# Performance work log

Hardware: AMD Instinct MI355X
Metric: run time of the kernel (lower is better)

The kernel has to match this reference:

```python
import jax, jax.numpy as jnp
import numpy as np

N = 50000      # nodes
E = 800000     # edges (avg degree 16)
C = 5000       # clusters (Kongming compression)
D = 128        # in_features
OUT = 40       # out_features (classes)
K = 2          # propagation hops


def setup_inputs() -> dict:
    key = jax.random.key(0)
    k1, k2, k3, k4, k5, k6 = jax.random.split(key, 6)
    x = jax.random.normal(k1, (N, D), dtype=jnp.float32)
    edge_index = jax.random.randint(k2, (2, E), 0, N, dtype=jnp.int32)
    cluster_index = jax.random.randint(k3, (N,), 0, C, dtype=jnp.int32)
    rep_idx = jax.random.randint(k4, (C,), 0, N, dtype=jnp.int32)
    W = jax.random.normal(k5, (OUT, D), dtype=jnp.float32) / np.sqrt(D)
    b = jax.random.normal(k6, (OUT,), dtype=jnp.float32) * 0.01
    return {"x": x, "edge_index": edge_index, "cluster_index": cluster_index,
            "rep_idx": rep_idx, "W": W, "b": b}


def _gcn_propagate(x, edge_index, k_hops):
    # PUPropagate: K hops of D^{-1/2}(A+I)D^{-1/2} x (gcn_norm with self-loops)
    n = x.shape[0]
    loops = jnp.arange(n, dtype=edge_index.dtype)
    src = jnp.concatenate([edge_index[0], loops])
    dst = jnp.concatenate([edge_index[1], loops])
    deg = jax.ops.segment_sum(jnp.ones_like(src, dtype=x.dtype), dst, num_segments=n)
    dinv = jnp.where(deg > 0, jax.lax.rsqrt(deg), 0.0)
    norm = (dinv[src] * dinv[dst])[:, None]            # [E+N, 1]
    h = x
    for _ in range(k_hops):                            # small fixed hop count
        h = jax.ops.segment_sum(h[src] * norm, dst, num_segments=n)
    return h


def reference(x, edge_index, cluster_index, rep_idx, W, b):
    h = _gcn_propagate(x, edge_index, K)               # [N, D]
    # Kongming_Cluster: gather one representative row per cluster
    hc = h[rep_idx]                                    # [C, D]
    yc = hc @ W.T + b                                  # [C, OUT] dense linear on compressed rows
    # Kongming_Reconstruct: scatter back to all nodes by cluster index
    y = yc[cluster_index]                              # [N, OUT]
    return jax.nn.log_softmax(y, axis=1)
```

## Files before the change

### kernel.cpp

```cpp
#include <hip/hip_runtime.h>
#include <math.h>

#define N_NODES 50000
#define N_EDGES 800000
#define N_CLUST 5000
#define DIM     128
#define NOUT    40
#define SLOTS   64
#define CSLOT   64

#define NBKT    391
#define BCAP    2560
#define GB_STR  16
#define BUCKB   250
#define EPB4    800

#define ZB     782
#define INVB   50
#define GRID_A (ZB + INVB + BUCKB)

typedef __attribute__((ext_vector_type(8))) short short8;
typedef __attribute__((ext_vector_type(4))) float fvec4;
typedef __attribute__((ext_vector_type(4))) int ivec4;
typedef __attribute__((ext_vector_type(4))) unsigned uvec4;

__device__ __forceinline__ short bf16r(float v) {
    unsigned u = __float_as_uint(v);
    u = (u + 0x7FFFu + ((u >> 16) & 1u)) >> 16;
    return (short)u;
}
__device__ __forceinline__ unsigned pack_bf16x2(float a, float b) {
    unsigned ua = __float_as_uint(a);
    unsigned ub = __float_as_uint(b);
    ua = (ua + 0x7FFFu + ((ua >> 16) & 1u)) >> 16;
    ub = (ub + 0x7FFFu + ((ub >> 16) & 1u)) >> 16;
    return ua | (ub << 16);
}
__device__ __forceinline__ float2 unpack_bf16x2(unsigned v) {
    float2 r;
    r.x = __uint_as_float(v << 16);
    r.y = __uint_as_float(v & 0xFFFF0000u);
    return r;
}
__device__ __forceinline__ float4 unpack_bf16x4(uint2 v) {
    float4 r;
    r.x = __uint_as_float(v.x << 16);
    r.y = __uint_as_float(v.x & 0xFFFF0000u);
    r.z = __uint_as_float(v.y << 16);
    r.w = __uint_as_float(v.y & 0xFFFF0000u);
    return r;
}
struct f8 { float4 a, b; };
__device__ __forceinline__ f8 unpack_bf16x8(uint4 q) {
    f8 r;
    r.a.x = __uint_as_float(q.x << 16);
    r.a.y = __uint_as_float(q.x & 0xFFFF0000u);
    r.a.z = __uint_as_float(q.y << 16);
    r.a.w = __uint_as_float(q.y & 0xFFFF0000u);
    r.b.x = __uint_as_float(q.z << 16);
    r.b.y = __uint_as_float(q.z & 0xFFFF0000u);
    r.b.z = __uint_as_float(q.w << 16);
    r.b.w = __uint_as_float(q.w & 0xFFFF0000u);
    return r;
}
__device__ __forceinline__ float4 sel4(bool c, float4 v) {
    float4 r;
    r.x = c ? v.x : 0.0f; r.y = c ? v.y : 0.0f;
    r.z = c ? v.z : 0.0f; r.w = c ? v.w : 0.0f;
    return r;
}

__global__ __launch_bounds__(256) void fused_A(const float* __restrict__ x,
                                               const int* __restrict__ esrc,
                                               const int* __restrict__ edst,
                                               const int* __restrict__ cidx,
                                               const float* __restrict__ W,
                                               int* __restrict__ ccnt,
                                               unsigned short* __restrict__ zs,
                                               unsigned short* __restrict__ cinv,
                                               int* __restrict__ gbcnt,
                                               unsigned* __restrict__ gbuck) {
    __shared__ int bcnt[NBKT];
    __shared__ int bbase[NBKT];
    int lane = threadIdx.x & 63;
    int wv = threadIdx.x >> 6;

    if (blockIdx.x < ZB) {
        int gw = blockIdx.x * 4 + wv;
        if (gw >= N_NODES / 16) return;
        int q = lane >> 4, r16 = lane & 15;

        short8 bfr[3][4];
        #pragma unroll
        for (int t = 0; t < 3; t++) {
            int o = t * 16 + r16;
            #pragma unroll
            for (int s = 0; s < 4; s++) {
                short8 f = {0, 0, 0, 0, 0, 0, 0, 0};
                if (o < NOUT) {
                    const float* wp = W + o * DIM + s * 32 + q * 8;
                    float4 w0 = *(const float4*)wp;
                    float4 w1 = *(const float4*)(wp + 4);
                    f[0] = bf16r(w0.x); f[1] = bf16r(w0.y);
                    f[2] = bf16r(w0.z); f[3] = bf16r(w0.w);
                    f[4] = bf16r(w1.x); f[5] = bf16r(w1.y);
                    f[6] = bf16r(w1.z); f[7] = bf16r(w1.w);
                }
                bfr[t][s] = f;
            }
        }

        int tile = gw;
        int node = tile * 16 + r16;
        short8 af[4];
        #pragma unroll
        for (int s = 0; s < 4; s++) {
            const fvec4* xp = (const fvec4*)(x + (size_t)node * DIM + s * 32 + q * 8);
            fvec4 a0 = *xp;
            fvec4 a1 = *(xp + 1);
            short8 f;
            f[0] = bf16r(a0.x); f[1] = bf16r(a0.y);
            f[2] = bf16r(a0.z); f[3] = bf16r(a0.w);
            f[4] = bf16r(a1.x); f[5] = bf16r(a1.y);
            f[6] = bf16r(a1.z); f[7] = bf16r(a1.w);
            af[s] = f;
        }

        fvec4 acc0 = {0, 0, 0, 0}, acc1 = {0, 0, 0, 0}, acc2 = {0, 0, 0, 0};
        #pragma unroll
        for (int s = 0; s < 4; s++) {
            acc0 = __builtin_amdgcn_mfma_f32_16x16x32_bf16(af[s], bfr[0][s], acc0, 0, 0, 0);
            acc1 = __builtin_amdgcn_mfma_f32_16x16x32_bf16(af[s], bfr[1][s], acc1, 0, 0, 0);
            acc2 = __builtin_amdgcn_mfma_f32_16x16x32_bf16(af[s], bfr[2][s], acc2, 0, 0, 0);
        }

        #pragma unroll
        for (int r = 0; r < 4; r++) {
            int nd = tile * 16 + q * 4 + r;
            unsigned short* zrow = zs + (size_t)nd * NOUT;
            zrow[r16] = (unsigned short)bf16r(acc0[r]);
            zrow[16 + r16] = (unsigned short)bf16r(acc1[r]);
            if (r16 < 8)
                zrow[32 + r16] = (unsigned short)bf16r(acc2[r]);
        }
    } else if (blockIdx.x < ZB + INVB) {
        int t0 = (blockIdx.x - ZB) * 256 + threadIdx.x;
        for (int i = t0; i < N_NODES; i += INVB * 256) {
            int c = cidx[i];
            int pos = atomicAdd(&ccnt[c], 1);
            if (pos < CSLOT) cinv[c * CSLOT + pos] = (unsigned short)i;
        }
    } else {
        int fb = blockIdx.x - ZB - INVB;
        const ivec4* src4 = (const ivec4*)esrc;
        const ivec4* dst4 = (const ivec4*)edst;
        int q0 = fb * EPB4;

        for (int i = threadIdx.x; i < NBKT; i += 256) bcnt[i] = 0;
        __syncthreads();

        for (int i = threadIdx.x; i < EPB4; i += 256) {
            ivec4 d4 = dst4[q0 + i];
            atomicAdd(&bcnt[d4.x >> 7], 1);
            atomicAdd(&bcnt[d4.y >> 7], 1);
            atomicAdd(&bcnt[d4.z >> 7], 1);
            atomicAdd(&bcnt[d4.w >> 7], 1);
        }
        __syncthreads();

        for (int bk = threadIdx.x; bk < NBKT; bk += 256) {
            int c = bcnt[bk];
            bbase[bk] = c ? atomicAdd(&gbcnt[bk * GB_STR], c) : 0;
        }
        __syncthreads();
        for (int i = threadIdx.x; i < NBKT; i += 256) bcnt[i] = 0;
        __syncthreads();

        for (int i = threadIdx.x; i < EPB4; i += 256) {
            ivec4 d4 = dst4[q0 + i];
            ivec4 s4 = src4[q0 + i];
            {
                int bk = d4.x >> 7; int idx = atomicAdd(&bcnt[bk], 1);
                unsigned p = (unsigned)(bbase[bk] + idx);
                if (p < BCAP) gbuck[(size_t)bk * BCAP + p] = ((unsigned)d4.x << 16) | (unsigned)s4.x;
            }
            {
                int bk = d4.y >> 7; int idx = atomicAdd(&bcnt[bk], 1);
                unsigned p = (unsigned)(bbase[bk] + idx);
                if (p < BCAP) gbuck[(size_t)bk * BCAP + p] = ((unsigned)d4.y << 16) | (unsigned)s4.y;
            }
            {
                int bk = d4.z >> 7; int idx = atomicAdd(&bcnt[bk], 1);
                unsigned p = (unsigned)(bbase[bk] + idx);
                if (p < BCAP) gbuck[(size_t)bk * BCAP + p] = ((unsigned)d4.z << 16) | (unsigned)s4.z;
            }
            {
                int bk = d4.w >> 7; int idx = atomicAdd(&bcnt[bk], 1);
                unsigned p = (unsigned)(bbase[bk] + idx);
                if (p < BCAP) gbuck[(size_t)bk * BCAP + p] = ((unsigned)d4.w << 16) | (unsigned)s4.w;
            }
        }
    }
}

__global__ __launch_bounds__(256) void build_scale(const unsigned* __restrict__ gbuck,
                                                   const int* __restrict__ gbcnt,
                                                   const uint2* __restrict__ zs2,
                                                   int* __restrict__ cnt,
                                                   unsigned short* __restrict__ slot,
                                                   uint2* __restrict__ zd2) {
    __shared__ int c128[128];
    __shared__ unsigned short sl[128 * SLOTS];
    int tid = threadIdx.x;
    int b = blockIdx.x;
    if (tid < 128) c128[tid] = 0;
    __syncthreads();
    int m = gbcnt[b * GB_STR];
    if (m > BCAP) m = BCAP;
    const unsigned* bk = gbuck + (size_t)b * BCAP;
    for (int i = tid; i < m; i += 256) {
        unsigned e = bk[i];
        int d7 = (int)(e >> 16) & 127;
        int pos = atomicAdd(&c128[d7], 1);
        if (pos < SLOTS) sl[(d7 << 6) + pos] = (unsigned short)(e & 0xFFFFu);
    }
    __syncthreads();
    {
        int rows = N_NODES - (b << 7);
        if (rows > 128) rows = 128;
        int n4 = rows * (SLOTS / 8);
        const uvec4* s4 = (const uvec4*)sl;
        uvec4* g4 = (uvec4*)(slot + ((size_t)(b << 7)) * SLOTS);
        for (int i = tid; i < n4; i += 256)
            g4[i] = s4[i];
    }
    int n0 = b << 7;
    if (tid < 128) {
        int n = n0 + tid;
        if (n < N_NODES) cnt[n] = c128[tid];
    }
    for (int i = tid; i < 128 * 10; i += 256) {
        int r = i / 10;
        int n = n0 + r;
        if (n < N_NODES) {
            int k = i - r * 10;
            float dn = rsqrtf((float)(c128[r] + 1));
            float4 f = unpack_bf16x4(zs2[(size_t)n * 10 + k]);
            uint2 p;
            p.x = pack_bf16x2(dn * f.x, dn * f.y);
            p.y = pack_bf16x2(dn * f.z, dn * f.w);
            zd2[(size_t)n * 10 + k] = p;
        }
    }
}

__global__ __launch_bounds__(256) void hop_all(const uint4* __restrict__ zd4,
                                               uint4* __restrict__ v14,
                                               const uint4* __restrict__ slot4,
                                               const int* __restrict__ cnt) {
    int lane = threadIdx.x & 63;
    int wv = threadIdx.x >> 6;
    int g = lane / 5;
    int k = lane - g * 5;
    int n = blockIdx.x * 48 + wv * 12 + g;
    if (g >= 12 || n >= N_NODES) return;
    int c = cnt[n];
    int m = (c < SLOTS) ? c : SLOTS;
    float s = 1.0f / (float)(c + 1);
    f8 self = unpack_bf16x8(zd4[(size_t)n * 5 + k]);
    float4 aA = self.a, aB = self.b;
    float4 bA = {0, 0, 0, 0}, bB = {0, 0, 0, 0};
    const uint4* srow = slot4 + (size_t)n * 8;
    int j = 0;
    for (; j + 8 <= m; j += 8) {
        uint4 s8 = srow[j >> 3];
        f8 f0 = unpack_bf16x8(zd4[(size_t)(s8.x & 0xFFFFu) * 5 + k]);
        f8 f1 = unpack_bf16x8(zd4[(size_t)(s8.x >> 16) * 5 + k]);
        f8 f2 = unpack_bf16x8(zd4[(size_t)(s8.y & 0xFFFFu) * 5 + k]);
        f8 f3 = unpack_bf16x8(zd4[(size_t)(s8.y >> 16) * 5 + k]);
        f8 f4 = unpack_bf16x8(zd4[(size_t)(s8.z & 0xFFFFu) * 5 + k]);
        f8 f5 = unpack_bf16x8(zd4[(size_t)(s8.z >> 16) * 5 + k]);
        f8 f6 = unpack_bf16x8(zd4[(size_t)(s8.w & 0xFFFFu) * 5 + k]);
        f8 f7 = unpack_bf16x8(zd4[(size_t)(s8.w >> 16) * 5 + k]);
        aA = aA + ((f0.a + f1.a) + (f4.a + f5.a));
        aB = aB + ((f0.b + f1.b) + (f4.b + f5.b));
        bA = bA + ((f2.a + f3.a) + (f6.a + f7.a));
        bB = bB + ((f2.b + f3.b) + (f6.b + f7.b));
    }
    if (j < m) {
        int rem = m - j;
        uint4 s8 = srow[j >> 3];
        unsigned i0 = s8.x & 0xFFFFu;
        unsigned i1 = (rem > 1) ? (s8.x >> 16) : 0u;
        unsigned i2 = (rem > 2) ? (s8.y & 0xFFFFu) : 0u;
        unsigned i3 = (rem > 3) ? (s8.y >> 16) : 0u;
        unsigned i4 = (rem > 4) ? (s8.z & 0xFFFFu) : 0u;
        unsigned i5 = (rem > 5) ? (s8.z >> 16) : 0u;
        unsigned i6 = (rem > 6) ? (s8.w & 0xFFFFu) : 0u;
        f8 f0 = unpack_bf16x8(zd4[(size_t)i0 * 5 + k]);
        f8 f1 = unpack_bf16x8(zd4[(size_t)i1 * 5 + k]);
        f8 f2 = unpack_bf16x8(zd4[(size_t)i2 * 5 + k]);
        f8 f3 = unpack_bf16x8(zd4[(size_t)i3 * 5 + k]);
        f8 f4 = unpack_bf16x8(zd4[(size_t)i4 * 5 + k]);
        f8 f5 = unpack_bf16x8(zd4[(size_t)i5 * 5 + k]);
        f8 f6 = unpack_bf16x8(zd4[(size_t)i6 * 5 + k]);
        aA = aA + f0.a;
        aB = aB + f0.b;
        bA = bA + sel4(rem > 1, f1.a) + sel4(rem > 3, f3.a) + sel4(rem > 5, f5.a);
        bB = bB + sel4(rem > 1, f1.b) + sel4(rem > 3, f3.b) + sel4(rem > 5, f5.b);
        aA = aA + sel4(rem > 2, f2.a) + sel4(rem > 4, f4.a) + sel4(rem > 6, f6.a);
        aB = aB + sel4(rem > 2, f2.b) + sel4(rem > 4, f4.b) + sel4(rem > 6, f6.b);
    }
    float4 rA = aA + bA;
    float4 rB = aB + bB;
    uint4 o;
    o.x = pack_bf16x2(s * rA.x, s * rA.y);
    o.y = pack_bf16x2(s * rA.z, s * rA.w);
    o.z = pack_bf16x2(s * rB.x, s * rB.y);
    o.w = pack_bf16x2(s * rB.z, s * rB.w);
    v14[(size_t)n * 5 + k] = o;
}

__global__ __launch_bounds__(256) void rep_scatter(const unsigned* __restrict__ v1,
                                                   const unsigned short* __restrict__ slot,
                                                   const int* __restrict__ cnt,
                                                   const int* __restrict__ ccnt,
                                                   const unsigned short* __restrict__ cinv,
                                                   const int* __restrict__ rep_idx,
                                                   const float2* __restrict__ b2,
                                                   float2* __restrict__ out2) {
    int lane = threadIdx.x & 63;
    int wv = threadIdx.x >> 6;
    int c = blockIdx.x * 4 + wv;
    if (c >= N_CLUST) return;
    int n = rep_idx[c];
    int cn = cnt[n];
    int m = (cn < SLOTS) ? cn : SLOTS;
    float dn = rsqrtf((float)(cn + 1));
    int g = lane / 20;
    int k = lane - g * 20;
    float2 acc; acc.x = 0.0f; acc.y = 0.0f;
    if (g == 0) acc = unpack_bf16x2(v1[n * 20 + k]);
    if (g < 3) {
        int base = n * SLOTS;
        for (int j = g; j < m; j += 3) {
            float2 f = unpack_bf16x2(v1[(int)slot[base + j] * 20 + k]);
            acc.x += f.x; acc.y += f.y;
        }
    }
    float t1x = __shfl(acc.x, lane + 20), t1y = __shfl(acc.y, lane + 20);
    float t2x = __shfl(acc.x, lane + 40), t2y = __shfl(acc.y, lane + 40);
    bool act = (lane < 20);
    float2 h; h.x = 0.0f; h.y = 0.0f;
    if (act) {
        float2 bb = b2[k];
        h.x = dn * (acc.x + t1x + t2x) + bb.x;
        h.y = dn * (acc.y + t1y + t2y) + bb.y;
    }
    float mx = act ? fmaxf(h.x, h.y) : -INFINITY;
    #pragma unroll
    for (int off = 32; off; off >>= 1) mx = fmaxf(mx, __shfl_xor(mx, off));
    float e = act ? (expf(h.x - mx) + expf(h.y - mx)) : 0.0f;
    #pragma unroll
    for (int off = 32; off; off >>= 1) e += __shfl_xor(e, off);
    float lg = mx + logf(e);
    float2 o; o.x = h.x - lg; o.y = h.y - lg;
    float ox = __shfl(o.x, k);
    float oy = __shfl(o.y, k);
    int mc = ccnt[c];
    if (mc > CSLOT) mc = CSLOT;
    const unsigned short* mem = cinv + c * CSLOT;
    if (g < 3) {
        float2 ob; ob.x = ox; ob.y = oy;
        for (int idx = g; idx < mc; idx += 3) {
            int node = (int)mem[idx];
            out2[(size_t)node * 20 + k] = ob;
        }
    }
}

extern "C" void kernel_launch(void* const* d_in, const int* in_sizes, int n_in,
                              void* d_out, int out_size, void* d_ws, size_t ws_size,
                              hipStream_t stream) {
    const float* x    = (const float*)d_in[0];
    const int*   esrc = (const int*)d_in[1];
    const int*   edst = ((const int*)d_in[1]) + N_EDGES;
    const int*   cidx = (const int*)d_in[2];
    const int*   ridx = (const int*)d_in[3];
    const float* W    = (const float*)d_in[4];
    const float* b    = (const float*)d_in[5];
    float* out = (float*)d_out;

    char* ws = (char*)d_ws;
    size_t off = 0;
    auto alloc = [&](size_t bytes) { char* p = ws + off; off += (bytes + 255) & ~size_t(255); return p; };
    int*            cnt   = (int*)alloc((N_NODES + N_CLUST + NBKT * GB_STR) * 4);
    int*            ccnt  = cnt + N_NODES;
    int*            gbcnt = ccnt + N_CLUST;
    unsigned short* slot  = (unsigned short*)alloc((size_t)N_NODES * SLOTS * 2);
    unsigned short* zs    = (unsigned short*)alloc((size_t)N_NODES * NOUT * 2);
    unsigned short* zd    = (unsigned short*)alloc((size_t)N_NODES * NOUT * 2);
    unsigned*       v1    = (unsigned*)alloc((size_t)N_NODES * (NOUT / 2) * 4);
    unsigned short* cinv  = (unsigned short*)alloc((size_t)N_CLUST * CSLOT * 2);
    unsigned*       gbuck = (unsigned*)alloc((size_t)NBKT * BCAP * 4);
    (void)ws_size; (void)in_sizes; (void)n_in; (void)out_size;

    (void)hipMemsetAsync(ccnt, 0, (N_CLUST + NBKT * GB_STR) * 4, stream);

    fused_A<<<GRID_A, 256, 0, stream>>>(x, esrc, edst, cidx, W,
                                        ccnt, zs, cinv, gbcnt, gbuck);
    build_scale<<<NBKT, 256, 0, stream>>>(gbuck, gbcnt, (const uint2*)zs,
                                          cnt, slot, (uint2*)zd);
    hop_all<<<(N_NODES + 47) / 48, 256, 0, stream>>>((const uint4*)zd, (uint4*)v1,
                                                     (const uint4*)slot, cnt);
    rep_scatter<<<(N_CLUST + 3) / 4, 256, 0, stream>>>((const unsigned*)v1, slot, cnt,
                                                       ccnt, cinv, ridx,
                                                       (const float2*)b, (float2*)out);
}
```

Before: 136.5 us.

## Replace global bucket atomics with per-block fixed segments in edge binning

The edge-binning phase no longer counts and then reserves space with global atomics. Each of 500 blocks instead writes its edges into private fixed-size segments (28 entries per bucket) together with a per-block count, so a single pass with no cross-block atomics suffices. build_scale then walks all 500 segments for its bucket, one thread per segment doing a serial loop. Block ordering is also changed so the binning and cluster-inverse blocks launch before the MFMA projection blocks. The risks are a larger, sparser workspace, uncoalesced serial segment reads in build_scale, and edges silently dropped if any segment overflows.

```diff
diff --git a/kernel.cpp b/kernel.cpp
--- a/kernel.cpp
+++ b/kernel.cpp
@@ -10,14 +10,15 @@
 #define CSLOT   64
 
 #define NBKT    391
-#define BCAP    2560
-#define GB_STR  16
-#define BUCKB   250
-#define EPB4    800
-
-#define ZB     782
-#define INVB   50
-#define GRID_A (ZB + INVB + BUCKB)
+#define BUCKB   500
+#define EPB4    400
+#define SEG     28
+
+#define INV0    BUCKB
+#define INVB    196
+#define ZG0     (INV0 + INVB)
+#define ZB      782
+#define GRID_A  (ZG0 + ZB)
 
 typedef __attribute__((ext_vector_type(8))) short short8;
 typedef __attribute__((ext_vector_type(4))) float fvec4;
@@ -78,15 +79,59 @@
                                                int* __restrict__ ccnt,
                                                unsigned short* __restrict__ zs,
                                                unsigned short* __restrict__ cinv,
-                                               int* __restrict__ gbcnt,
+                                               int* __restrict__ gcount,
                                                unsigned* __restrict__ gbuck) {
     __shared__ int bcnt[NBKT];
-    __shared__ int bbase[NBKT];
     int lane = threadIdx.x & 63;
     int wv = threadIdx.x >> 6;
 
-    if (blockIdx.x < ZB) {
-        int gw = blockIdx.x * 4 + wv;
+    if (blockIdx.x < BUCKB) {
+        int fb = blockIdx.x;
+        const ivec4* src4 = (const ivec4*)esrc;
+        const ivec4* dst4 = (const ivec4*)edst;
+        int q0 = fb * EPB4;
+
+        for (int i = threadIdx.x; i < NBKT; i += 256) bcnt[i] = 0;
+        __syncthreads();
+
+        for (int i = threadIdx.x; i < EPB4; i += 256) {
+            ivec4 d4 = dst4[q0 + i];
+            ivec4 s4 = src4[q0 + i];
+            {
+                int bk = d4.x >> 7; int pos = atomicAdd(&bcnt[bk], 1);
+                if (pos < SEG) gbuck[((size_t)fb * NBKT + bk) * SEG + pos] =
+                                   ((unsigned)d4.x << 16) | (unsigned)s4.x;
+            }
+            {
+                int bk = d4.y >> 7; int pos = atomicAdd(&bcnt[bk], 1);
+                if (pos < SEG) gbuck[((size_t)fb * NBKT + bk) * SEG + pos] =
+                                   ((unsigned)d4.y << 16) | (unsigned)s4.y;
+            }
+            {
+                int bk = d4.z >> 7; int pos = atomicAdd(&bcnt[bk], 1);
+                if (pos < SEG) gbuck[((size_t)fb * NBKT + bk) * SEG + pos] =
+                                   ((unsigned)d4.z << 16) | (unsigned)s4.z;
+            }
+            {
+                int bk = d4.w >> 7; int pos = atomicAdd(&bcnt[bk], 1);
+                if (pos < SEG) gbuck[((size_t)fb * NBKT + bk) * SEG + pos] =
+                                   ((unsigned)d4.w << 16) | (unsigned)s4.w;
+            }
+        }
+        __syncthreads();
+        for (int bk = threadIdx.x; bk < NBKT; bk += 256) {
+            int c = bcnt[bk];
+            gcount[fb * NBKT + bk] = (c < SEG) ? c : SEG;
+        }
+    } else if (blockIdx.x < ZG0) {
+        int i = (blockIdx.x - INV0) * 256 + threadIdx.x;
+        if (i < N_NODES) {
+            int c = cidx[i];
+            int pos = atomicAdd(&ccnt[c], 1);
+            if (pos < CSLOT) cinv[c * CSLOT + pos] = (unsigned short)i;
+        }
+    } else {
+        int gw = (blockIdx.x - ZG0) * 4 + wv;
         if (gw >= N_NODES / 16) return;
         int q = lane >> 4, r16 = lane & 15;
 
@@ -143,68 +188,11 @@
             if (r16 < 8)
                 zrow[32 + r16] = (unsigned short)bf16r(acc2[r]);
         }
-    } else if (blockIdx.x < ZB + INVB) {
-        int t0 = (blockIdx.x - ZB) * 256 + threadIdx.x;
-        for (int i = t0; i < N_NODES; i += INVB * 256) {
-            int c = cidx[i];
-            int pos = atomicAdd(&ccnt[c], 1);
-            if (pos < CSLOT) cinv[c * CSLOT + pos] = (unsigned short)i;
-        }
-    } else {
-        int fb = blockIdx.x - ZB - INVB;
-        const ivec4* src4 = (const ivec4*)esrc;
-        const ivec4* dst4 = (const ivec4*)edst;
-        int q0 = fb * EPB4;
-
-        for (int i = threadIdx.x; i < NBKT; i += 256) bcnt[i] = 0;
-        __syncthreads();
-
-        for (int i = threadIdx.x; i < EPB4; i += 256) {
-            ivec4 d4 = dst4[q0 + i];
-            atomicAdd(&bcnt[d4.x >> 7], 1);
-            atomicAdd(&bcnt[d4.y >> 7], 1);
-            atomicAdd(&bcnt[d4.z >> 7], 1);
-            atomicAdd(&bcnt[d4.w >> 7], 1);
-        }
-        __syncthreads();
-
-        for (int bk = threadIdx.x; bk < NBKT; bk += 256) {
-            int c = bcnt[bk];
-            bbase[bk] = c ? atomicAdd(&gbcnt[bk * GB_STR], c) : 0;
-        }
-        __syncthreads();
-        for (int i = threadIdx.x; i < NBKT; i += 256) bcnt[i] = 0;
-        __syncthreads();
-
-        for (int i = threadIdx.x; i < EPB4; i += 256) {
-            ivec4 d4 = dst4[q0 + i];
-            ivec4 s4 = src4[q0 + i];
-            {
-                int bk = d4.x >> 7; int idx = atomicAdd(&bcnt[bk], 1);
-                unsigned p = (unsigned)(bbase[bk] + idx);
-                if (p < BCAP) gbuck[(size_t)bk * BCAP + p] = ((unsigned)d4.x << 16) | (unsigned)s4.x;
-            }
-            {
-                int bk = d4.y >> 7; int idx = atomicAdd(&bcnt[bk], 1);
-                unsigned p = (unsigned)(bbase[bk] + idx);
-                if (p < BCAP) gbuck[(size_t)bk * BCAP + p] = ((unsigned)d4.y << 16) | (unsigned)s4.y;
-            }
-            {
-                int bk = d4.z >> 7; int idx = atomicAdd(&bcnt[bk], 1);
-                unsigned p = (unsigned)(bbase[bk] + idx);
-                if (p < BCAP) gbuck[(size_t)bk * BCAP + p] = ((unsigned)d4.z << 16) | (unsigned)s4.z;
-            }
-            {
-                int bk = d4.w >> 7; int idx = atomicAdd(&bcnt[bk], 1);
-                unsigned p = (unsigned)(bbase[bk] + idx);
-                if (p < BCAP) gbuck[(size_t)bk * BCAP + p] = ((unsigned)d4.w << 16) | (unsigned)s4.w;
-            }
-        }
     }
 }
 
 __global__ __launch_bounds__(256) void build_scale(const unsigned* __restrict__ gbuck,
-                                                   const int* __restrict__ gbcnt,
+                                                   const int* __restrict__ gcount,
                                                    const uint2* __restrict__ zs2,
                                                    int* __restrict__ cnt,
                                                    unsigned short* __restrict__ slot,
@@ -215,14 +203,15 @@
     int b = blockIdx.x;
     if (tid < 128) c128[tid] = 0;
     __syncthreads();
-    int m = gbcnt[b * GB_STR];
-    if (m > BCAP) m = BCAP;
-    const unsigned* bk = gbuck + (size_t)b * BCAP;
-    for (int i = tid; i < m; i += 256) {
-        unsigned e = bk[i];
-        int d7 = (int)(e >> 16) & 127;
-        int pos = atomicAdd(&c128[d7], 1);
-        if (pos < SLOTS) sl[(d7 << 6) + pos] = (unsigned short)(e & 0xFFFFu);
+    for (int sb = tid; sb < BUCKB; sb += 256) {
+        int m = gcount[sb * NBKT + b];
+        const unsigned* seg = gbuck + ((size_t)sb * NBKT + b) * SEG;
+        for (int i = 0; i < m; i++) {
+            unsigned e = seg[i];
+            int d7 = (int)(e >> 16) & 127;
+            int pos = atomicAdd(&c128[d7], 1);
+            if (pos < SLOTS) sl[(d7 << 6) + pos] = (unsigned short)(e & 0xFFFFu);
+        }
     }
     __syncthreads();
     {
@@ -394,22 +383,22 @@
     char* ws = (char*)d_ws;
     size_t off = 0;
     auto alloc = [&](size_t bytes) { char* p = ws + off; off += (bytes + 255) & ~size_t(255); return p; };
-    int*            cnt   = (int*)alloc((N_NODES + N_CLUST + NBKT * GB_STR) * 4);
-    int*            ccnt  = cnt + N_NODES;
-    int*            gbcnt = ccnt + N_CLUST;
-    unsigned short* slot  = (unsigned short*)alloc((size_t)N_NODES * SLOTS * 2);
-    unsigned short* zs    = (unsigned short*)alloc((size_t)N_NODES * NOUT * 2);
-    unsigned short* zd    = (unsigned short*)alloc((size_t)N_NODES * NOUT * 2);
-    unsigned*       v1    = (unsigned*)alloc((size_t)N_NODES * (NOUT / 2) * 4);
-    unsigned short* cinv  = (unsigned short*)alloc((size_t)N_CLUST * CSLOT * 2);
-    unsigned*       gbuck = (unsigned*)alloc((size_t)NBKT * BCAP * 4);
+    int*            cnt    = (int*)alloc((N_NODES + N_CLUST) * 4);
+    int*            ccnt   = cnt + N_NODES;
+    int*            gcount = (int*)alloc((size_t)BUCKB * NBKT * 4);
+    unsigned short* slot   = (unsigned short*)alloc((size_t)N_NODES * SLOTS * 2);
+    unsigned short* zs     = (unsigned short*)alloc((size_t)N_NODES * NOUT * 2);
+    unsigned short* zd     = (unsigned short*)alloc((size_t)N_NODES * NOUT * 2);
+    unsigned*       v1     = (unsigned*)alloc((size_t)N_NODES * (NOUT / 2) * 4);
+    unsigned short* cinv   = (unsigned short*)alloc((size_t)N_CLUST * CSLOT * 2);
+    unsigned*       gbuck  = (unsigned*)alloc((size_t)BUCKB * NBKT * SEG * 4);
     (void)ws_size; (void)in_sizes; (void)n_in; (void)out_size;
 
-    (void)hipMemsetAsync(ccnt, 0, (N_CLUST + NBKT * GB_STR) * 4, stream);
+    (void)hipMemsetAsync(ccnt, 0, N_CLUST * 4, stream);
 
     fused_A<<<GRID_A, 256, 0, stream>>>(x, esrc, edst, cidx, W,
-                                        ccnt, zs, cinv, gbcnt, gbuck);
-    build_scale<<<NBKT, 256, 0, stream>>>(gbuck, gbcnt, (const uint2*)zs,
+                                        ccnt, zs, cinv, gcount, gbuck);
+    build_scale<<<NBKT, 256, 0, stream>>>(gbuck, gcount, (const uint2*)zs,
                                           cnt, slot, (uint2*)zd);
     hop_all<<<(N_NODES + 47) / 48, 256, 0, stream>>>((const uint4*)zd, (uint4*)v1,
                                                      (const uint4*)slot, cnt);
```

Result: slower. 139.7 us (+2.3%).
